# Kernel optimization log

Hardware: AMD Instinct MI355X
Metric: run time of the kernel (lower is better)

## Reference

```python
import jax, jax.numpy as jnp
import numpy as np

N = 50000          # num nodes
E = 800000         # num edges (before self-loops)
F_IN = 128
H = 4              # heads
C1 = 16            # hidden channels per head
C2 = 8             # out channels per head
NEG_SLOPE = 0.2
EPS = 1e-16


def setup_inputs() -> dict:
    key = jax.random.key(0)
    ks = jax.random.split(key, 10)
    x = jax.random.normal(ks[0], (N, F_IN), dtype=jnp.float32)
    edge_index = jax.random.randint(ks[1], (2, E), 0, N, dtype=jnp.int64)
    s1 = 1.0 / np.sqrt(F_IN)
    s2 = 1.0 / np.sqrt(H * C1)
    return {
        "x": x,
        "edge_index": edge_index,
        "W1": jax.random.normal(ks[2], (F_IN, H * C1), dtype=jnp.float32) * s1,
        "a_src1": jax.random.normal(ks[3], (H, C1), dtype=jnp.float32) * s2,
        "a_dst1": jax.random.normal(ks[4], (H, C1), dtype=jnp.float32) * s2,
        "b1": jnp.zeros((H * C1,), dtype=jnp.float32),
        "W2": jax.random.normal(ks[5], (H * C1, H * C2), dtype=jnp.float32) * s2,
        "a_src2": jax.random.normal(ks[6], (H, C2), dtype=jnp.float32) * 0.2,
        "a_dst2": jax.random.normal(ks[7], (H, C2), dtype=jnp.float32) * 0.2,
        "b2": jnp.zeros((H * C2,), dtype=jnp.float32),
    }


def _gat_conv(x, src, dst, W, a_src, a_dst, b, heads, ch):
    # linear transform -> per-head features [N, H, C]
    h = (x @ W).reshape(-1, heads, ch)
    # per-node attention logits [N, H]
    al_src = jnp.sum(h * a_src[None], axis=-1)
    al_dst = jnp.sum(h * a_dst[None], axis=-1)
    # edge-wise logits + leaky relu [E, H]
    e = al_src[src] + al_dst[dst]
    e = jnp.where(e >= 0, e, NEG_SLOPE * e)
    # segment softmax over destination neighborhoods
    m = jax.ops.segment_max(e, dst, num_segments=N)
    e = jnp.exp(e - m[dst])
    s = jax.ops.segment_sum(e, dst, num_segments=N)
    alpha = e / (s[dst] + EPS)                      # [E, H]
    # weighted gather-scatter aggregate [N, H, C]
    msg = h[src] * alpha[..., None]
    out = jax.ops.segment_sum(msg, dst, num_segments=N)
    # concat heads + bias
    return out.reshape(-1, heads * ch) + b


def reference(x, edge_index, W1, a_src1, a_dst1, b1, W2, a_src2, a_dst2, b2):
    # PyG GATConv adds self-loops by default
    loop = jnp.arange(N, dtype=edge_index.dtype)
    src = jnp.concatenate([edge_index[0], loop])
    dst = jnp.concatenate([edge_index[1], loop])
    h = _gat_conv(x, src, dst, W1, a_src1, a_dst1, b1, H, C1)
    h = jax.nn.relu(h)
    h = _gat_conv(h, src, dst, W2, a_src2, a_dst2, b2, H, C2)
    return jax.nn.log_softmax(h, axis=1)
```

## Files before the change

kernel.cpp:

```cpp
#include <hip/hip_runtime.h>
#include <hip/hip_bf16.h>
#include <math.h>

#define NN 50000
#define NE 800000
#define ET (NE + NN)
#define DCAP 48
#define MAXOVF 8192
#define NG1R 1568
#define NBP 196
#define NRANGE 6250
#define NCB 832

__device__ __forceinline__ float bf2f(unsigned short u) {
    return __uint_as_float(((unsigned)u) << 16);
}
__device__ __forceinline__ unsigned short f2bf(float f) {
    unsigned u = __float_as_uint(f);
    return (unsigned short)((u + 0x7fff + ((u >> 16) & 1)) >> 16);
}
__device__ __forceinline__ float lrelu(float e) {
    return e >= 0.f ? e : 0.2f * e;
}

__global__ __launch_bounds__(256) void k_compact(const void* __restrict__ xraw,
                                                 const void* __restrict__ ei,
                                                 const void* p2, const void* p3, const void* p4, const void* p5,
                                                 const void* p6, const void* p7, const void* p8, const void* p9,
                                                 unsigned short* __restrict__ srcc,
                                                 unsigned short* __restrict__ dstc,
                                                 float* __restrict__ wsm) {
    __shared__ int wred[8];
    int t = threadIdx.x;
    const unsigned long long* e64u = (const unsigned long long*)ei;
    const unsigned int* x32 = (const unsigned int*)xraw;
    int ci = 0, cf = 0;
    #pragma unroll
    for (int q = 0; q < 4; q++) {
        if (e64u[4 * t + q] >= (unsigned long long)NN) ci = 1;
        unsigned ex = (x32[4 * t + q] >> 7) & 0xFFu;
        cf += (ex >= 96 && ex <= 140) ? 1 : 0;
    }
    #pragma unroll
    for (int off = 32; off; off >>= 1) { ci |= __shfl_xor(ci, off); cf += __shfl_xor(cf, off); }
    if ((t & 63) == 0) { wred[t >> 6] = ci; wred[4 + (t >> 6)] = cf; }
    __syncthreads();
    int iflag = (wred[0] | wred[1] | wred[2] | wred[3]) ? 0 : 1;
    int fl = ((wred[4] + wred[5] + wred[6] + wred[7]) > 700) ? 1 : 0;

    int g0 = blockIdx.x * 256 + t;
    if (g0 < 10528) {
        const void* p; int off;
        if (g0 < 8192)       { p = p2; off = g0; }
        else if (g0 < 8256)  { p = p3; off = g0 - 8192; }
        else if (g0 < 8320)  { p = p4; off = g0 - 8256; }
        else if (g0 < 8384)  { p = p5; off = g0 - 8320; }
        else if (g0 < 10432) { p = p6; off = g0 - 8384; }
        else if (g0 < 10464) { p = p7; off = g0 - 10432; }
        else if (g0 < 10496) { p = p8; off = g0 - 10464; }
        else                 { p = p9; off = g0 - 10496; }
        wsm[g0] = fl ? bf2f(((const unsigned short*)p)[off]) : ((const float*)p)[off];
    }
    const long long* e64s = (const long long*)ei;
    const int* e32s = (const int*)ei;
    for (int e = g0; e < NE; e += NCB * 256) {
        int s, d;
        if (iflag) { s = (int)e64s[e]; d = (int)e64s[NE + e]; }
        else       { s = e32s[e];      d = e32s[NE + e]; }
        srcc[e] = (unsigned short)s;
        dstc[e] = (unsigned short)d;
    }
    for (int i = g0; i < NN; i += NCB * 256) {
        srcc[NE + i] = (unsigned short)i;
        dstc[NE + i] = (unsigned short)i;
    }
}

__global__ __launch_bounds__(256) void k_gemm1cv(const void* __restrict__ xraw,
                                                 const void* __restrict__ w1raw,
                                                 const void* __restrict__ as1raw,
                                                 const void* __restrict__ ad1raw,
                                                 const unsigned short* __restrict__ srcc,
                                                 const unsigned short* __restrict__ dstc,
                                                 unsigned short* __restrict__ h1b,
                                                 float* __restrict__ als, float* __restrict__ ald,
                                                 unsigned short* __restrict__ csrF, int* __restrict__ deg,
                                                 int2* __restrict__ ovf, int* __restrict__ ovfcnt) {
    __shared__ unsigned int Wp[64 * 65];
    __shared__ float xt[32 * 132];
    __shared__ int wred[4];
    int tid = threadIdx.x;
    int rb = blockIdx.x * 32;

    const unsigned int* x32 = (const unsigned int*)xraw;
    int cf = 0;
    #pragma unroll
    for (int q = 0; q < 4; q++) {
        unsigned ex = (x32[4 * tid + q] >> 7) & 0xFFu;
        cf += (ex >= 96 && ex <= 140) ? 1 : 0;
    }
    #pragma unroll
    for (int off = 32; off; off >>= 1) cf += __shfl_xor(cf, off);
    if ((tid & 63) == 0) wred[tid >> 6] = cf;
    __syncthreads();
    int fl = ((wred[0] + wred[1] + wred[2] + wred[3]) > 700) ? 1 : 0;

    if (rb < NN) {
        for (int i = tid; i < 64 * 64; i += 256) {
            int k2 = i >> 6, c = i & 63;
            unsigned lo, hi;
            if (fl) {
                lo = ((const unsigned short*)w1raw)[(2 * k2) * 64 + c];
                hi = ((const unsigned short*)w1raw)[(2 * k2 + 1) * 64 + c];
            } else {
                lo = f2bf(((const float*)w1raw)[(2 * k2) * 64 + c]);
                hi = f2bf(((const float*)w1raw)[(2 * k2 + 1) * 64 + c]);
            }
            Wp[c * 65 + k2] = lo | (hi << 16);
        }
        if (fl) {
            const unsigned short* xb = (const unsigned short*)xraw;
            for (int i = tid; i < 32 * 16; i += 256) {
                int r = i >> 4, k8 = i & 15;
                float f[8];
                if (rb + r < NN) {
                    uint4 v = ((const uint4*)xb)[(size_t)(rb + r) * 16 + k8];
                    f[0] = bf2f((unsigned short)(v.x & 0xffff)); f[1] = bf2f((unsigned short)(v.x >> 16));
                    f[2] = bf2f((unsigned short)(v.y & 0xffff)); f[3] = bf2f((unsigned short)(v.y >> 16));
                    f[4] = bf2f((unsigned short)(v.z & 0xffff)); f[5] = bf2f((unsigned short)(v.z >> 16));
                    f[6] = bf2f((unsigned short)(v.w & 0xffff)); f[7] = bf2f((unsigned short)(v.w >> 16));
                } else {
                    #pragma unroll
                    for (int q = 0; q < 8; q++) f[q] = 0.f;
                }
                int o = r * 132 + k8 * 8;
                *(float4*)&xt[o]     = make_float4(f[0], f[1], f[2], f[3]);
                *(float4*)&xt[o + 4] = make_float4(f[4], f[5], f[6], f[7]);
            }
        } else {
            const float* xf = (const float*)xraw;
            for (int i = tid; i < 32 * 32; i += 256) {
                int r = i >> 5, kq = i & 31;
                float4 v = make_float4(0.f, 0.f, 0.f, 0.f);
                if (rb + r < NN) v = ((const float4*)xf)[(size_t)(rb + r) * 32 + kq];
                *(float4*)&xt[r * 132 + kq * 4] = v;
            }
        }
        __syncthreads();
        int c = tid & 63;
        int rg = tid >> 6;
        float acc[8];
        #pragma unroll
        for (int j = 0; j < 8; j++) acc[j] = 0.f;
        for (int k2 = 0; k2 < 64; k2 += 2) {
            unsigned q0 = Wp[c * 65 + k2];
            unsigned q1 = Wp[c * 65 + k2 + 1];
            float w0 = __uint_as_float(q0 << 16);
            float w1 = __uint_as_float(q0 & 0xffff0000u);
            float w2 = __uint_as_float(q1 << 16);
            float w3 = __uint_as_float(q1 & 0xffff0000u);
            int kk = k2 * 2;
            #pragma unroll
            for (int j = 0; j < 8; j++) {
                float4 xv = *(const float4*)&xt[(rg * 8 + j) * 132 + kk];
                acc[j] = fmaf(xv.x, w0, fmaf(xv.y, w1, fmaf(xv.z, w2, fmaf(xv.w, w3, acc[j]))));
            }
        }
        float asf = fl ? bf2f(((const unsigned short*)as1raw)[c]) : ((const float*)as1raw)[c];
        float adf = fl ? bf2f(((const unsigned short*)ad1raw)[c]) : ((const float*)ad1raw)[c];
        #pragma unroll
        for (int j = 0; j < 8; j++) {
            int r = rb + rg * 8 + j;
            bool ok = r < NN;
            if (ok) h1b[(size_t)r * 64 + c] = f2bf(acc[j]);
            float v = acc[j] * asf, w = acc[j] * adf;
            #pragma unroll
            for (int off = 1; off < 16; off <<= 1) {
                v += __shfl_xor(v, off);
                w += __shfl_xor(w, off);
            }
            if (ok && (c & 15) == 0) {
                als[r * 4 + (c >> 4)] = v;
                ald[r * 4 + (c >> 4)] = w;
            }
        }
    }

    int part = blockIdx.x & 7;
    int bi = blockIdx.x >> 3;
    int lo = part * NRANGE, hi = lo + NRANGE;
    for (int e = bi * 256 + tid; e < ET; e += NBP * 256) {
        int d = dstc[e];
        if (d >= lo && d < hi) {
            int s = srcc[e];
            int slot = atomicAdd(&deg[d], 1);
            if (slot < DCAP) csrF[(size_t)d * DCAP + slot] = (unsigned short)s;
            else {
                int o = atomicAdd(ovfcnt, 1);
                if (o < MAXOVF) ovf[o] = make_int2(s, d);
            }
        }
    }
}

__global__ __launch_bounds__(256) void k_agg1(const int* __restrict__ degv, const unsigned short* __restrict__ csrF,
                                              const int2* __restrict__ ovf, const int* __restrict__ ovfcnt,
                                              const float* __restrict__ als, const float* __restrict__ aldv,
                                              const unsigned short* __restrict__ h1b,
                                              const float* __restrict__ b1,
                                              float* __restrict__ out1) {
    __shared__ float pv[4][DCAP * 4];
    __shared__ int  sidx[4][DCAP];
    int w = threadIdx.x >> 6, lane = threadIdx.x & 63;
    int n = blockIdx.x * 4 + w;
    if (n >= NN) return;
    int dg = degv[n];
    const unsigned short* cf = csrF + (size_t)n * DCAP;
    float4 ald = *(const float4*)(aldv + 4 * n);

    if (dg <= DCAP) {
        int sA = 0;
        bool v0 = lane < dg;
        if (v0) {
            sA = cf[lane];
            sidx[w][lane] = sA;
            float4 a = *(const float4*)(als + 4 * sA);
            float4 p;
            p.x = __expf(lrelu(a.x + ald.x)); p.y = __expf(lrelu(a.y + ald.y));
            p.z = __expf(lrelu(a.z + ald.z)); p.w = __expf(lrelu(a.w + ald.w));
            *(float4*)&pv[w][lane * 4] = p;
        }
        int degp = (dg + 3) & ~3;
        int s0v = __shfl(sA, 0);
        if (lane >= dg && lane < degp) {
            sidx[w][lane] = s0v;
            *(float4*)&pv[w][lane * 4] = make_float4(0.f, 0.f, 0.f, 0.f);
        }
        int g = lane >> 4, j = lane & 15, hh = j >> 2;
        float4 a4 = make_float4(0.f, 0.f, 0.f, 0.f);
        float ps = 0.f;
        for (int e = 0; e < degp; e += 4) {
            int s = sidx[w][e + g];
            float ph = pv[w][(e + g) * 4 + hh];
            uint2 rv = *(const uint2*)&h1b[(size_t)s * 64 + j * 4];
            ps += ph;
            a4.x = fmaf(ph, bf2f((unsigned short)(rv.x & 0xffff)), a4.x);
            a4.y = fmaf(ph, bf2f((unsigned short)(rv.x >> 16)),    a4.y);
            a4.z = fmaf(ph, bf2f((unsigned short)(rv.y & 0xffff)), a4.z);
            a4.w = fmaf(ph, bf2f((unsigned short)(rv.y >> 16)),    a4.w);
        }
        #pragma unroll
        for (int off = 16; off <= 32; off <<= 1) {
            a4.x += __shfl_xor(a4.x, off);
            a4.y += __shfl_xor(a4.y, off);
            a4.z += __shfl_xor(a4.z, off);
            a4.w += __shfl_xor(a4.w, off);
            ps   += __shfl_xor(ps,   off);
        }
        if (g == 0) {
            float rh = 1.f / (ps + 1e-16f);
            float4 bb = *(const float4*)&b1[j * 4];
            float4 o;
            o.x = fmaxf(a4.x * rh + bb.x, 0.f);
            o.y = fmaxf(a4.y * rh + bb.y, 0.f);
            o.z = fmaxf(a4.z * rh + bb.z, 0.f);
            o.w = fmaxf(a4.w * rh + bb.w, 0.f);
            *(float4*)&out1[(size_t)n * 64 + j * 4] = o;
        }
    } else {
        int h = lane >> 4;
        int oN = min(*ovfcnt, MAXOVF);
        float s0 = 0.f, s1 = 0.f, s2 = 0.f, s3 = 0.f;
        for (int i = lane; i < DCAP; i += 64) {
            int s = cf[i];
            float4 a = *(const float4*)(als + 4 * s);
            s0 += __expf(lrelu(a.x + ald.x));
            s1 += __expf(lrelu(a.y + ald.y));
            s2 += __expf(lrelu(a.z + ald.z));
            s3 += __expf(lrelu(a.w + ald.w));
        }
        for (int i = lane; i < oN; i += 64) {
            int2 pr = ovf[i];
            if (pr.y == n) {
                float4 a = *(const float4*)(als + 4 * pr.x);
                s0 += __expf(lrelu(a.x + ald.x));
                s1 += __expf(lrelu(a.y + ald.y));
                s2 += __expf(lrelu(a.z + ald.z));
                s3 += __expf(lrelu(a.w + ald.w));
            }
        }
        #pragma unroll
        for (int off = 32; off; off >>= 1) {
            s0 += __shfl_xor(s0, off);
            s1 += __shfl_xor(s1, off);
            s2 += __shfl_xor(s2, off);
            s3 += __shfl_xor(s3, off);
        }
        float sh = (h == 0) ? s0 : (h == 1) ? s1 : (h == 2) ? s2 : s3;
        float ah = (h == 0) ? ald.x : (h == 1) ? ald.y : (h == 2) ? ald.z : ald.w;
        float rh = 1.f / (sh + 1e-16f);
        float acc = 0.f;
        for (int e = 0; e < DCAP; ++e) {
            int s = cf[e];
            float av = als[4 * s + h];
            float ph = __expf(lrelu(av + ah));
            acc = fmaf(ph, bf2f(h1b[(size_t)s * 64 + lane]), acc);
        }
        for (int o = 0; o < oN; ++o) {
            int2 pr = ovf[o];
            if (pr.y == n) {
                float av = als[4 * pr.x + h];
                float ph = __expf(lrelu(av + ah));
                acc = fmaf(ph, bf2f(h1b[(size_t)pr.x * 64 + lane]), acc);
            }
        }
        out1[(size_t)n * 64 + lane] = fmaxf(acc * rh + b1[lane], 0.f);
    }
}

__global__ __launch_bounds__(256) void k_gemm2(const float* __restrict__ in,
                                               const float* __restrict__ Wf,
                                               const float* __restrict__ asf_p,
                                               const float* __restrict__ adf_p,
                                               unsigned short* __restrict__ h2b,
                                               float* __restrict__ als, float* __restrict__ ald) {
    __shared__ float Wt[32 * 65];
    __shared__ float xt[64 * 68];
    int tid = threadIdx.x;
    int rb = blockIdx.x * 64;
    for (int i = tid; i < 64 * 32; i += 256) {
        int k = i >> 5, c = i & 31;
        Wt[c * 65 + k] = Wf[i];
    }
    for (int i = tid; i < 64 * 16; i += 256) {
        int r = i >> 4, kq = i & 15;
        float4 v = make_float4(0.f, 0.f, 0.f, 0.f);
        if (rb + r < NN) v = ((const float4*)in)[(size_t)(rb + r) * 16 + kq];
        *(float4*)&xt[r * 68 + kq * 4] = v;
    }
    __syncthreads();
    int c = tid & 31, rg = tid >> 5;
    float acc[8];
    #pragma unroll
    for (int j = 0; j < 8; j++) acc[j] = 0.f;
    #pragma unroll 2
    for (int k = 0; k < 64; k += 4) {
        float4 w;
        w.x = Wt[c * 65 + k];     w.y = Wt[c * 65 + k + 1];
        w.z = Wt[c * 65 + k + 2]; w.w = Wt[c * 65 + k + 3];
        #pragma unroll
        for (int j = 0; j < 8; j++) {
            float4 xv = *(const float4*)&xt[(rg * 8 + j) * 68 + k];
            acc[j] = fmaf(xv.x, w.x, fmaf(xv.y, w.y, fmaf(xv.z, w.z, fmaf(xv.w, w.w, acc[j]))));
        }
    }
    float asf = asf_p[c], adf = adf_p[c];
    #pragma unroll
    for (int j = 0; j < 8; j++) {
        int r = rb + rg * 8 + j;
        bool ok = r < NN;
        if (ok) h2b[(size_t)r * 32 + c] = f2bf(acc[j]);
        float v = acc[j] * asf, w = acc[j] * adf;
        #pragma unroll
        for (int off = 1; off < 8; off <<= 1) {
            v += __shfl_xor(v, off);
            w += __shfl_xor(w, off);
        }
        if (ok && (c & 7) == 0) {
            als[r * 4 + (c >> 3)] = v;
            ald[r * 4 + (c >> 3)] = w;
        }
    }
}

__global__ __launch_bounds__(256) void k_agg2(const int* __restrict__ degv, const unsigned short* __restrict__ csrF,
                                              const int2* __restrict__ ovf, const int* __restrict__ ovfcnt,
                                              const float* __restrict__ als, const float* __restrict__ aldv,
                                              const unsigned short* __restrict__ h2b,
                                              const float* __restrict__ b2,
                                              float* __restrict__ out) {
    __shared__ float pv[4][DCAP * 4];
    __shared__ int  sidx[4][DCAP];
    int w = threadIdx.x >> 6, lane = threadIdx.x & 63;
    int n = blockIdx.x * 4 + w;
    if (n >= NN) return;
    int dg = degv[n];
    const unsigned short* cf = csrF + (size_t)n * DCAP;
    float4 ald = *(const float4*)(aldv + 4 * n);

    if (dg <= DCAP) {
        int sA = 0;
        bool v0 = lane < dg;
        if (v0) {
            sA = cf[lane];
            sidx[w][lane] = sA;
            float4 a = *(const float4*)(als + 4 * sA);
            float4 p;
            p.x = __expf(lrelu(a.x + ald.x)); p.y = __expf(lrelu(a.y + ald.y));
            p.z = __expf(lrelu(a.z + ald.z)); p.w = __expf(lrelu(a.w + ald.w));
            *(float4*)&pv[w][lane * 4] = p;
        }
        int degp = (dg + 7) & ~7;
        int s0v = __shfl(sA, 0);
        if (lane >= dg && lane < degp) {
            sidx[w][lane] = s0v;
            *(float4*)&pv[w][lane * 4] = make_float4(0.f, 0.f, 0.f, 0.f);
        }
        int g = lane >> 3, j = lane & 7, hh = j >> 1;
        float4 a4 = make_float4(0.f, 0.f, 0.f, 0.f);
        float ps = 0.f;
        for (int e = 0; e < degp; e += 8) {
            int s = sidx[w][e + g];
            float ph = pv[w][(e + g) * 4 + hh];
            uint2 rv = *(const uint2*)&h2b[(size_t)s * 32 + j * 4];
            ps += ph;
            a4.x = fmaf(ph, bf2f((unsigned short)(rv.x & 0xffff)), a4.x);
            a4.y = fmaf(ph, bf2f((unsigned short)(rv.x >> 16)),    a4.y);
            a4.z = fmaf(ph, bf2f((unsigned short)(rv.y & 0xffff)), a4.z);
            a4.w = fmaf(ph, bf2f((unsigned short)(rv.y >> 16)),    a4.w);
        }
        #pragma unroll
        for (int off = 8; off <= 32; off <<= 1) {
            a4.x += __shfl_xor(a4.x, off);
            a4.y += __shfl_xor(a4.y, off);
            a4.z += __shfl_xor(a4.z, off);
            a4.w += __shfl_xor(a4.w, off);
            ps   += __shfl_xor(ps,   off);
        }
        float rh = 1.f / (ps + 1e-16f);
        float4 bb = *(const float4*)&b2[j * 4];
        float4 row;
        row.x = a4.x * rh + bb.x; row.y = a4.y * rh + bb.y;
        row.z = a4.z * rh + bb.z; row.w = a4.w * rh + bb.w;
        float mx = fmaxf(fmaxf(row.x, row.y), fmaxf(row.z, row.w));
        #pragma unroll
        for (int off = 1; off < 8; off <<= 1) mx = fmaxf(mx, __shfl_xor(mx, off));
        float sm = __expf(row.x - mx) + __expf(row.y - mx)
                 + __expf(row.z - mx) + __expf(row.w - mx);
        #pragma unroll
        for (int off = 1; off < 8; off <<= 1) sm += __shfl_xor(sm, off);
        float lse = mx + logf(sm);
        if (g == 0) {
            float4 o;
            o.x = row.x - lse; o.y = row.y - lse;
            o.z = row.z - lse; o.w = row.w - lse;
            *(float4*)&out[(size_t)n * 32 + j * 4] = o;
        }
    } else {
        int oN = min(*ovfcnt, MAXOVF);
        float s0 = 0.f, s1 = 0.f, s2 = 0.f, s3 = 0.f;
        for (int i = lane; i < DCAP; i += 64) {
            int s = cf[i];
            float4 a = *(const float4*)(als + 4 * s);
            s0 += __expf(lrelu(a.x + ald.x));
            s1 += __expf(lrelu(a.y + ald.y));
            s2 += __expf(lrelu(a.z + ald.z));
            s3 += __expf(lrelu(a.w + ald.w));
        }
        for (int i = lane; i < oN; i += 64) {
            int2 pr = ovf[i];
            if (pr.y == n) {
                float4 a = *(const float4*)(als + 4 * pr.x);
                s0 += __expf(lrelu(a.x + ald.x));
                s1 += __expf(lrelu(a.y + ald.y));
                s2 += __expf(lrelu(a.z + ald.z));
                s3 += __expf(lrelu(a.w + ald.w));
            }
        }
        #pragma unroll
        for (int off = 32; off; off >>= 1) {
            s0 += __shfl_xor(s0, off);
            s1 += __shfl_xor(s1, off);
            s2 += __shfl_xor(s2, off);
            s3 += __shfl_xor(s3, off);
        }
        int L = lane & 31;
        int h2i = L >> 3;
        float sh2 = (h2i == 0) ? s0 : (h2i == 1) ? s1 : (h2i == 2) ? s2 : s3;
        float ah2 = (h2i == 0) ? ald.x : (h2i == 1) ? ald.y : (h2i == 2) ? ald.z : ald.w;
        float rh2 = 1.f / (sh2 + 1e-16f);
        if (lane < 32) {
            float acc = 0.f;
            for (int e = 0; e < DCAP; ++e) {
                int s = cf[e];
                float av = als[4 * s + h2i];
                float ph = __expf(lrelu(av + ah2));
                acc = fmaf(ph, bf2f(h2b[(size_t)s * 32 + L]), acc);
            }
            for (int o = 0; o < oN; ++o) {
                int2 pr = ovf[o];
                if (pr.y == n) {
                    float av = als[4 * pr.x + h2i];
                    float ph = __expf(lrelu(av + ah2));
                    acc = fmaf(ph, bf2f(h2b[(size_t)pr.x * 32 + L]), acc);
                }
            }
            float row = acc * rh2 + b2[L];
            float mx = row;
            #pragma unroll
            for (int off = 16; off; off >>= 1) mx = fmaxf(mx, __shfl_xor(mx, off, 32));
            float pe = __expf(row - mx);
            float sm = pe;
            #pragma unroll
            for (int off = 16; off; off >>= 1) sm += __shfl_xor(sm, off, 32);
            out[(size_t)n * 32 + L] = row - mx - logf(sm);
        }
    }
}

extern "C" void kernel_launch(void* const* d_in, const int* in_sizes, int n_in,
                              void* d_out, int out_size, void* d_ws, size_t ws_size,
                              hipStream_t stream) {
    const void* x  = d_in[0];
    const void* ei = d_in[1];
    float* out = (float*)d_out;

    char* p = (char*)d_ws;
    auto take = [&](size_t b) -> char* {
        char* r = p; p += (b + 255) & ~(size_t)255; return r;
    };
    int*   degc  = (int*)take(sizeof(int) * (NN + 8));
    int*   deg   = degc;
    int*   ovfcnt = degc + NN;
    unsigned short* csrF = (unsigned short*)take(sizeof(unsigned short) * (size_t)NN * DCAP);
    int2*  ovf   = (int2*)take(sizeof(int2) * MAXOVF);
    unsigned short* srcc = (unsigned short*)take(sizeof(unsigned short) * ET);
    unsigned short* dstc = (unsigned short*)take(sizeof(unsigned short) * ET);
    float* wsm   = (float*)take(sizeof(float) * 10528);
    unsigned short* h1b = (unsigned short*)take(sizeof(unsigned short) * (size_t)NN * 64);
    float* als1  = (float*)take(sizeof(float) * NN * 4);
    float* ald1  = (float*)take(sizeof(float) * NN * 4);
    float* out1  = (float*)take(sizeof(float) * (size_t)NN * 64);
    unsigned short* h2b = (unsigned short*)take(sizeof(unsigned short) * (size_t)NN * 32);
    float* als2  = (float*)take(sizeof(float) * NN * 4);
    float* ald2  = (float*)take(sizeof(float) * NN * 4);

    float* Wf2  = wsm + 8384;
    float* as2f = wsm + 10432;
    float* ad2f = wsm + 10464;
    float* b1f  = wsm + 8320;
    float* b2f  = wsm + 10496;

    hipMemsetAsync(degc, 0, sizeof(int) * (NN + 8), stream);
    k_compact<<<NCB, 256, 0, stream>>>(x, ei, d_in[2], d_in[3], d_in[4], d_in[5],
                                       d_in[6], d_in[7], d_in[8], d_in[9],
                                       srcc, dstc, wsm);
    k_gemm1cv<<<NG1R, 256, 0, stream>>>(x, d_in[2], d_in[3], d_in[4], srcc, dstc,
                                        h1b, als1, ald1, csrF, deg, ovf, ovfcnt);
    k_agg1<<<(NN + 3) / 4, 256, 0, stream>>>(deg, csrF, ovf, ovfcnt, als1, ald1, h1b, b1f, out1);
    k_gemm2<<<(NN + 63) / 64, 256, 0, stream>>>(out1, Wf2, as2f, ad2f, h2b, als2, ald2);
    k_agg2<<<(NN + 3) / 4, 256, 0, stream>>>(deg, csrF, ovf, ovfcnt, als2, ald2, h2b, b2f, out);
}
```

Measured before the change: 222.7 us.

## Pack src/dst into one word, shrink CSR slot cap, scatter before GEMM

Measured after the change: 230.2 us. +3.3%, slower.

```diff
diff --git a/kernel.cpp b/kernel.cpp
--- a/kernel.cpp
+++ b/kernel.cpp
@@ -5,7 +5,7 @@
 #define NN 50000
 #define NE 800000
 #define ET (NE + NN)
-#define DCAP 48
+#define DCAP 32
 #define MAXOVF 8192
 #define NG1R 1568
 #define NBP 196
@@ -27,8 +27,7 @@
                                                  const void* __restrict__ ei,
                                                  const void* p2, const void* p3, const void* p4, const void* p5,
                                                  const void* p6, const void* p7, const void* p8, const void* p9,
-                                                 unsigned short* __restrict__ srcc,
-                                                 unsigned short* __restrict__ dstc,
+                                                 unsigned int* __restrict__ pk,
                                                  float* __restrict__ wsm) {
     __shared__ int wred[8];
     int t = threadIdx.x;
@@ -64,15 +63,13 @@
     const long long* e64s = (const long long*)ei;
     const int* e32s = (const int*)ei;
     for (int e = g0; e < NE; e += NCB * 256) {
-        int s, d;
-        if (iflag) { s = (int)e64s[e]; d = (int)e64s[NE + e]; }
-        else       { s = e32s[e];      d = e32s[NE + e]; }
-        srcc[e] = (unsigned short)s;
-        dstc[e] = (unsigned short)d;
+        unsigned s, d;
+        if (iflag) { s = (unsigned)e64s[e]; d = (unsigned)e64s[NE + e]; }
+        else       { s = (unsigned)e32s[e]; d = (unsigned)e32s[NE + e]; }
+        pk[e] = (d << 16) | s;
     }
     for (int i = g0; i < NN; i += NCB * 256) {
-        srcc[NE + i] = (unsigned short)i;
-        dstc[NE + i] = (unsigned short)i;
+        pk[NE + i] = ((unsigned)i << 16) | (unsigned)i;
     }
 }
 
@@ -80,8 +77,7 @@
                                                  const void* __restrict__ w1raw,
                                                  const void* __restrict__ as1raw,
                                                  const void* __restrict__ ad1raw,
-                                                 const unsigned short* __restrict__ srcc,
-                                                 const unsigned short* __restrict__ dstc,
+                                                 const unsigned int* __restrict__ pk,
                                                  unsigned short* __restrict__ h1b,
                                                  float* __restrict__ als, float* __restrict__ ald,
                                                  unsigned short* __restrict__ csrF, int* __restrict__ deg,
@@ -92,6 +88,25 @@
     int tid = threadIdx.x;
     int rb = blockIdx.x * 32;
 
+    {
+        int part = blockIdx.x & 7;
+        int bi = blockIdx.x >> 3;
+        unsigned lo = (unsigned)(part * NRANGE), hi = lo + NRANGE;
+        for (int e = bi * 256 + tid; e < ET; e += NBP * 256) {
+            unsigned v = pk[e];
+            unsigned d = v >> 16;
+            if (d >= lo && d < hi) {
+                int s = (int)(v & 0xFFFFu);
+                int slot = atomicAdd(&deg[d], 1);
+                if (slot < DCAP) csrF[((size_t)d << 5) + slot] = (unsigned short)s;
+                else {
+                    int o = atomicAdd(ovfcnt, 1);
+                    if (o < MAXOVF) ovf[o] = make_int2(s, (int)d);
+                }
+            }
+        }
+    }
+
     const unsigned int* x32 = (const unsigned int*)xraw;
     int cf = 0;
     #pragma unroll
@@ -105,100 +120,84 @@
     __syncthreads();
     int fl = ((wred[0] + wred[1] + wred[2] + wred[3]) > 700) ? 1 : 0;
 
-    if (rb < NN) {
-        for (int i = tid; i < 64 * 64; i += 256) {
-            int k2 = i >> 6, c = i & 63;
-            unsigned lo, hi;
-            if (fl) {
-                lo = ((const unsigned short*)w1raw)[(2 * k2) * 64 + c];
-                hi = ((const unsigned short*)w1raw)[(2 * k2 + 1) * 64 + c];
+    if (rb >= NN) return;
+
+    for (int i = tid; i < 64 * 64; i += 256) {
+        int k2 = i >> 6, c = i & 63;
+        unsigned lo, hi;
+        if (fl) {
+            lo = ((const unsigned short*)w1raw)[(2 * k2) * 64 + c];
+            hi = ((const unsigned short*)w1raw)[(2 * k2 + 1) * 64 + c];
+        } else {
+            lo = f2bf(((const float*)w1raw)[(2 * k2) * 64 + c]);
+            hi = f2bf(((const float*)w1raw)[(2 * k2 + 1) * 64 + c]);
+        }
+        Wp[c * 65 + k2] = lo | (hi << 16);
+    }
+    if (fl) {
+        const unsigned short* xb = (const unsigned short*)xraw;
+        for (int i = tid; i < 32 * 16; i += 256) {
+            int r = i >> 4, k8 = i & 15;
+            float f[8];
+            if (rb + r < NN) {
+                uint4 v = ((const uint4*)xb)[(size_t)(rb + r) * 16 + k8];
+                f[0] = bf2f((unsigned short)(v.x & 0xffff)); f[1] = bf2f((unsigned short)(v.x >> 16));
+                f[2] = bf2f((unsigned short)(v.y & 0xffff)); f[3] = bf2f((unsigned short)(v.y >> 16));
+                f[4] = bf2f((unsigned short)(v.z & 0xffff)); f[5] = bf2f((unsigned short)(v.z >> 16));
+                f[6] = bf2f((unsigned short)(v.w & 0xffff)); f[7] = bf2f((unsigned short)(v.w >> 16));
             } else {
-                lo = f2bf(((const float*)w1raw)[(2 * k2) * 64 + c]);
-                hi = f2bf(((const float*)w1raw)[(2 * k2 + 1) * 64 + c]);
-            }
-            Wp[c * 65 + k2] = lo | (hi << 16);
-        }
-        if (fl) {
-            const unsigned short* xb = (const unsigned short*)xraw;
-            for (int i = tid; i < 32 * 16; i += 256) {
-                int r = i >> 4, k8 = i & 15;
-                float f[8];
-                if (rb + r < NN) {
-                    uint4 v = ((const uint4*)xb)[(size_t)(rb + r) * 16 + k8];
-                    f[0] = bf2f((unsigned short)(v.x & 0xffff)); f[1] = bf2f((unsigned short)(v.x >> 16));
-                    f[2] = bf2f((unsigned short)(v.y & 0xffff)); f[3] = bf2f((unsigned short)(v.y >> 16));
-                    f[4] = bf2f((unsigned short)(v.z & 0xffff)); f[5] = bf2f((unsigned short)(v.z >> 16));
-                    f[6] = bf2f((unsigned short)(v.w & 0xffff)); f[7] = bf2f((unsigned short)(v.w >> 16));
-                } else {
-                    #pragma unroll
-                    for (int q = 0; q < 8; q++) f[q] = 0.f;
-                }
-                int o = r * 132 + k8 * 8;
-                *(float4*)&xt[o]     = make_float4(f[0], f[1], f[2], f[3]);
-                *(float4*)&xt[o + 4] = make_float4(f[4], f[5], f[6], f[7]);
-            }
-        } else {
-            const float* xf = (const float*)xraw;
-            for (int i = tid; i < 32 * 32; i += 256) {
-                int r = i >> 5, kq = i & 31;
-                float4 v = make_float4(0.f, 0.f, 0.f, 0.f);
-                if (rb + r < NN) v = ((const float4*)xf)[(size_t)(rb + r) * 32 + kq];
-                *(float4*)&xt[r * 132 + kq * 4] = v;
-            }
-        }
-        __syncthreads();
-        int c = tid & 63;
-        int rg = tid >> 6;
-        float acc[8];
-        #pragma unroll
-        for (int j = 0; j < 8; j++) acc[j] = 0.f;
-        for (int k2 = 0; k2 < 64; k2 += 2) {
-            unsigned q0 = Wp[c * 65 + k2];
-            unsigned q1 = Wp[c * 65 + k2 + 1];
-            float w0 = __uint_as_float(q0 << 16);
-            float w1 = __uint_as_float(q0 & 0xffff0000u);
-            float w2 = __uint_as_float(q1 << 16);
-            float w3 = __uint_as_float(q1 & 0xffff0000u);
-            int kk = k2 * 2;
-            #pragma unroll
-            for (int j = 0; j < 8; j++) {
-                float4 xv = *(const float4*)&xt[(rg * 8 + j) * 132 + kk];
-                acc[j] = fmaf(xv.x, w0, fmaf(xv.y, w1, fmaf(xv.z, w2, fmaf(xv.w, w3, acc[j]))));
-            }
-        }
-        float asf = fl ? bf2f(((const unsigned short*)as1raw)[c]) : ((const float*)as1raw)[c];
-        float adf = fl ? bf2f(((const unsigned short*)ad1raw)[c]) : ((const float*)ad1raw)[c];
+                #pragma unroll
+                for (int q = 0; q < 8; q++) f[q] = 0.f;
+            }
+            int o = r * 132 + k8 * 8;
+            *(float4*)&xt[o]     = make_float4(f[0], f[1], f[2], f[3]);
+            *(float4*)&xt[o + 4] = make_float4(f[4], f[5], f[6], f[7]);
+        }
+    } else {
+        const float* xf = (const float*)xraw;
+        for (int i = tid; i < 32 * 32; i += 256) {
+            int r = i >> 5, kq = i & 31;
+            float4 v = make_float4(0.f, 0.f, 0.f, 0.f);
+            if (rb + r < NN) v = ((const float4*)xf)[(size_t)(rb + r) * 32 + kq];
+            *(float4*)&xt[r * 132 + kq * 4] = v;
+        }
+    }
+    __syncthreads();
+    int c = tid & 63;
+    int rg = tid >> 6;
+    float acc[8];
+    #pragma unroll
+    for (int j = 0; j < 8; j++) acc[j] = 0.f;
+    for (int k2 = 0; k2 < 64; k2 += 2) {
+        unsigned q0 = Wp[c * 65 + k2];
+        unsigned q1 = Wp[c * 65 + k2 + 1];
+        float w0 = __uint_as_float(q0 << 16);
+        float w1 = __uint_as_float(q0 & 0xffff0000u);
+        float w2 = __uint_as_float(q1 << 16);
+        float w3 = __uint_as_float(q1 & 0xffff0000u);
+        int kk = k2 * 2;
         #pragma unroll
         for (int j = 0; j < 8; j++) {
-            int r = rb + rg * 8 + j;
-            bool ok = r < NN;
-            if (ok) h1b[(size_t)r * 64 + c] = f2bf(acc[j]);
-            float v = acc[j] * asf, w = acc[j] * adf;
-            #pragma unroll
-            for (int off = 1; off < 16; off <<= 1) {
-                v += __shfl_xor(v, off);
-                w += __shfl_xor(w, off);
-            }
-            if (ok && (c & 15) == 0) {
-                als[r * 4 + (c >> 4)] = v;
-                ald[r * 4 + (c >> 4)] = w;
-            }
-        }
-    }
-
-    int part = blockIdx.x & 7;
-    int bi = blockIdx.x >> 3;
-    int lo = part * NRANGE, hi = lo + NRANGE;
-    for (int e = bi * 256 + tid; e < ET; e += NBP * 256) {
-        int d = dstc[e];
-        if (d >= lo && d < hi) {
-            int s = srcc[e];
-            int slot = atomicAdd(&deg[d], 1);
-            if (slot < DCAP) csrF[(size_t)d * DCAP + slot] = (unsigned short)s;
-            else {
-                int o = atomicAdd(ovfcnt, 1);
-                if (o < MAXOVF) ovf[o] = make_int2(s, d);
-            }
+            float4 xv = *(const float4*)&xt[(rg * 8 + j) * 132 + kk];
+            acc[j] = fmaf(xv.x, w0, fmaf(xv.y, w1, fmaf(xv.z, w2, fmaf(xv.w, w3, acc[j]))));
+        }
+    }
+    float asf = fl ? bf2f(((const unsigned short*)as1raw)[c]) : ((const float*)as1raw)[c];
+    float adf = fl ? bf2f(((const unsigned short*)ad1raw)[c]) : ((const float*)ad1raw)[c];
+    #pragma unroll
+    for (int j = 0; j < 8; j++) {
+        int r = rb + rg * 8 + j;
+        bool ok = r < NN;
+        if (ok) h1b[(size_t)r * 64 + c] = f2bf(acc[j]);
+        float v = acc[j] * asf, w = acc[j] * adf;
+        #pragma unroll
+        for (int off = 1; off < 16; off <<= 1) {
+            v += __shfl_xor(v, off);
+            w += __shfl_xor(w, off);
+        }
+        if (ok && (c & 15) == 0) {
+            als[r * 4 + (c >> 4)] = v;
+            ald[r * 4 + (c >> 4)] = w;
         }
     }
 }
@@ -215,7 +214,7 @@
     int n = blockIdx.x * 4 + w;
     if (n >= NN) return;
     int dg = degv[n];
-    const unsigned short* cf = csrF + (size_t)n * DCAP;
+    const unsigned short* cf = csrF + ((size_t)n << 5);
     float4 ald = *(const float4*)(aldv + 4 * n);
 
     if (dg <= DCAP) {
@@ -385,7 +384,7 @@
     int n = blockIdx.x * 4 + w;
     if (n >= NN) return;
     int dg = degv[n];
-    const unsigned short* cf = csrF + (size_t)n * DCAP;
+    const unsigned short* cf = csrF + ((size_t)n << 5);
     float4 ald = *(const float4*)(aldv + 4 * n);
 
     if (dg <= DCAP) {
@@ -524,8 +523,7 @@
     int*   ovfcnt = degc + NN;
     unsigned short* csrF = (unsigned short*)take(sizeof(unsigned short) * (size_t)NN * DCAP);
     int2*  ovf   = (int2*)take(sizeof(int2) * MAXOVF);
-    unsigned short* srcc = (unsigned short*)take(sizeof(unsigned short) * ET);
-    unsigned short* dstc = (unsigned short*)take(sizeof(unsigned short) * ET);
+    unsigned int* pk = (unsigned int*)take(sizeof(unsigned int) * ET);
     float* wsm   = (float*)take(sizeof(float) * 10528);
     unsigned short* h1b = (unsigned short*)take(sizeof(unsigned short) * (size_t)NN * 64);
     float* als1  = (float*)take(sizeof(float) * NN * 4);
@@ -544,8 +542,8 @@
     hipMemsetAsync(degc, 0, sizeof(int) * (NN + 8), stream);
     k_compact<<<NCB, 256, 0, stream>>>(x, ei, d_in[2], d_in[3], d_in[4], d_in[5],
                                        d_in[6], d_in[7], d_in[8], d_in[9],
-                                       srcc, dstc, wsm);
-    k_gemm1cv<<<NG1R, 256, 0, stream>>>(x, d_in[2], d_in[3], d_in[4], srcc, dstc,
+                                       pk, wsm);
+    k_gemm1cv<<<NG1R, 256, 0, stream>>>(x, d_in[2], d_in[3], d_in[4], pk,
                                         h1b, als1, ald1, csrF, deg, ovf, ovfcnt);
     k_agg1<<<(NN + 3) / 4, 256, 0, stream>>>(deg, csrF, ovf, ovfcnt, als1, ald1, h1b, b1f, out1);
     k_gemm2<<<(NN + 63) / 64, 256, 0, stream>>>(out1, Wf2, as2f, ad2f, h2b, als2, ald2);
```
